# Kernel optimization log

Measured on AMD Instinct MI355X. Metric: run time of the kernel, lower is better.

## Reference

```python
import jax, jax.numpy as jnp
import numpy as np

ALPHA = 300.0   # attractor_alpha
N_ATT = 16      # n_attractors
MIN_D = 0.001
MAX_D = 10.0


def _resize_bilinear_ac(x, out_h, out_w):
    """Bilinear resize with align_corners=True on trailing (H, W) dims of [B,C,h,w]."""
    h, w = x.shape[-2], x.shape[-1]
    ys = jnp.arange(out_h, dtype=jnp.float32) * ((h - 1) / max(out_h - 1, 1))
    xs = jnp.arange(out_w, dtype=jnp.float32) * ((w - 1) / max(out_w - 1, 1))
    y0 = jnp.floor(ys).astype(jnp.int32); y1 = jnp.minimum(y0 + 1, h - 1)
    x0 = jnp.floor(xs).astype(jnp.int32); x1 = jnp.minimum(x0 + 1, w - 1)
    wy = (ys - y0.astype(jnp.float32))[:, None]   # [out_h, 1]
    wx = (xs - x0.astype(jnp.float32))[None, :]   # [1, out_w]
    v00 = x[..., y0[:, None], x0[None, :]]
    v01 = x[..., y0[:, None], x1[None, :]]
    v10 = x[..., y1[:, None], x0[None, :]]
    v11 = x[..., y1[:, None], x1[None, :]]
    top = v00 * (1 - wx) + v01 * wx
    bot = v10 * (1 - wx) + v11 * wx
    return top * (1 - wy) + bot * wy


def setup_inputs() -> dict:
    key = jax.random.key(0)
    k = jax.random.split(key, 7)
    B, C, H, W = 4, 128, 192, 192
    n_bins = 64
    x = jax.random.normal(k[0], (B, C, H, W), dtype=jnp.float32)
    prev_bin = jax.random.uniform(k[1], (B, n_bins, H // 2, W // 2), dtype=jnp.float32)
    prev_bin_embedding = jax.random.normal(k[2], (B, C, H // 2, W // 2), dtype=jnp.float32)
    w1 = jax.random.normal(k[3], (128, 128), dtype=jnp.float32) * 0.05
    b1 = jnp.zeros((128,), dtype=jnp.float32)
    w2 = jax.random.normal(k[4], (2 * N_ATT, 128), dtype=jnp.float32) * 0.05
    b2 = jnp.zeros((2 * N_ATT,), dtype=jnp.float32)
    return {"x": x, "prev_bin": prev_bin, "prev_bin_embedding": prev_bin_embedding,
            "w1": w1, "b1": b1, "w2": w2, "b2": b2}


def reference(x, prev_bin, prev_bin_embedding, w1, b1, w2, b2):
    B, C, H, W = x.shape
    # add (interpolated) previous bin embedding
    pe = _resize_bilinear_ac(prev_bin_embedding, H, W)
    h = x + pe
    # per-pixel MLP (two 1x1 convs)
    h = jax.nn.relu(jnp.einsum('bchw,oc->bohw', h, w1) + b1[:, None, None])
    att = jax.nn.relu(jnp.einsum('bchw,oc->bohw', h, w2) + b2[:, None, None]) + 0.001
    # [B, n_attractors, 2, H, W] -> take normed attractor points
    att = att.reshape(B, N_ATT, 2, H, W)[:, :, 0]          # [B, nA, H, W]
    # upsample previous bin centers to feature resolution
    bc = _resize_bilinear_ac(prev_bin, H, W)               # [B, nB, H, W]
    # broadcast-subtract + inverse attractor + mean over attractors
    dx = att[:, :, None, :, :] - bc[:, None, :, :, :]      # [B, nA, nB, H, W]
    delta_c = jnp.mean(dx / (1.0 + ALPHA * dx * dx), axis=1)  # gamma = 2
    bin_new_centers = bc + delta_c
    bin_centers = (MAX_D - MIN_D) * bin_new_centers + MIN_D
    bin_centers = jnp.clip(jnp.sort(bin_centers, axis=1), MIN_D, MAX_D)
    return bin_new_centers, bin_centers
```

## Files before the change

kernel.cpp:

```cpp
#include <hip/hip_runtime.h>

constexpr int Bc = 4, Cc = 128, Hc = 192, Wc = 192;
constexpr int HI = 96, WI = 96;
constexpr int NB = 64;
constexpr int NA = 16;
constexpr float SCL = 95.0f / 191.0f;

typedef __attribute__((ext_vector_type(8))) short bf16x8;
typedef __attribute__((ext_vector_type(4))) float f32x4;

__device__ __forceinline__ unsigned short f2bf(float f) {
  unsigned u = __builtin_bit_cast(unsigned, f);
  unsigned r = (u + 0x7FFFu + ((u >> 16) & 1u)) >> 16;
  return (unsigned short)r;
}
__device__ __forceinline__ float rcp_fast(float r) {
#if defined(__has_builtin)
#if __has_builtin(__builtin_amdgcn_rcpf)
  return __builtin_amdgcn_rcpf(r);
#else
  return 1.0f / r;
#endif
#else
  return 1.0f / r;
#endif
}

__global__ __launch_bounds__(256) void k_prep(
    const float* __restrict__ w1, const float* __restrict__ w2,
    unsigned short* __restrict__ w1p, unsigned short* __restrict__ w2p)
{
  const int t = blockIdx.x * 256 + threadIdx.x;
  if (t < 16384) {
    const int e  = t & 7;
    const int l  = (t >> 3) & 63;
    const int kt = (t >> 9) & 3;
    const int nt = t >> 11;
    const int n  = nt * 16 + (l & 15);
    const int k  = kt * 32 + (l >> 4) * 8 + e;
    w1p[t] = f2bf(w1[n * 128 + k]);
  } else {
    const int u  = t - 16384;
    const int e  = u & 7;
    const int l  = (u >> 3) & 63;
    const int kt = u >> 9;
    const int n  = 2 * (l & 15);
    const int k  = kt * 32 + (l >> 4) * 8 + e;
    w2p[u] = f2bf(w2[n * 128 + k]);
  }
}

__global__ __launch_bounds__(256, 4) void k_att(
    const float* __restrict__ x, const float* __restrict__ pbe,
    const unsigned short* __restrict__ w1p, const float* __restrict__ b1,
    const unsigned short* __restrict__ w2p, const float* __restrict__ b2,
    float* __restrict__ att)
{
  constexpr int PH = 136;
  constexpr int RP = 37;
  __shared__ __align__(16) unsigned char smem[16384 + 128 * RP * 4];
  unsigned short* w1_s  = (unsigned short*)smem;
  float*          row_s = (float*)(smem + 16384);
  unsigned short* a1_s  = (unsigned short*)(smem + 16384);

  const int tid = threadIdx.x;
  const int xg0 = blockIdx.x * 64;
  const int y = blockIdx.y;
  const int b = blockIdx.z;

  const float ysf = y * SCL;
  const int y0 = (int)ysf;
  const int y1 = min(y0 + 1, HI - 1);
  const float wy = ysf - (float)y0;
  const int xi0 = (int)(xg0 * SCL);

  const int lane = tid & 63;
  const int wv = tid >> 6;
  const int ln = lane & 15;
  const int qd = lane >> 4;
  const int m0 = wv * 16;

  const int xg = xg0 + m0 + ln;
  const float xsf = (float)xg * SCL;
  const int x0i = (int)xsf;
  const float wx = xsf - (float)x0i;
  const int xl = x0i - xi0;

  float4 wstageA[4];
  {
    const float4* wp4 = (const float4*)w1p;
    #pragma unroll
    for (int i = 0; i < 4; ++i) wstageA[i] = wp4[tid + 256 * i];
  }

  float xr[32];
  #pragma unroll
  for (int kt = 0; kt < 4; ++kt) {
    #pragma unroll
    for (int j = 0; j < 8; ++j) {
      const int c = kt * 32 + qd * 8 + j;
      xr[kt * 8 + j] = x[((size_t)(b * Cc + c) * Hc + y) * Wc + xg];
    }
  }

  #pragma unroll
  for (int i = 0; i < 18; ++i) {
    const int f = tid + 256 * i;
    const int c = f / 36;
    const int xi = f - c * 36;
    const int xgl = min(xi0 + xi, WI - 1);
    const float* p = pbe + (size_t)(b * Cc + c) * (HI * WI);
    const float top = p[y0 * WI + xgl];
    const float bot = p[y1 * WI + xgl];
    row_s[c * RP + xi] = top + wy * (bot - top);
  }

  {
    float4* ws4 = (float4*)w1_s;
    #pragma unroll
    for (int i = 0; i < 4; ++i) ws4[tid + 256 * i] = wstageA[i];
  }
  __syncthreads();

  bf16x8 af[4];
  #pragma unroll
  for (int kt = 0; kt < 4; ++kt) {
    #pragma unroll
    for (int j = 0; j < 8; ++j) {
      const int c = kt * 32 + qd * 8 + j;
      const float v0 = row_s[c * RP + xl];
      const float v1 = row_s[c * RP + xl + 1];
      af[kt][j] = (short)f2bf(xr[kt * 8 + j] + v0 + wx * (v1 - v0));
    }
  }
  __syncthreads();

  float4 wstageB[4];
  {
    const float4* wp4 = (const float4*)w1p;
    #pragma unroll
    for (int i = 0; i < 4; ++i) wstageB[i] = wp4[1024 + tid + 256 * i];
  }
  float bias1[8];
  #pragma unroll
  for (int nt = 0; nt < 8; ++nt) bias1[nt] = b1[nt * 16 + ln];

  f32x4 acc[8];
  #pragma unroll
  for (int nt = 0; nt < 8; ++nt) acc[nt] = f32x4{0.f, 0.f, 0.f, 0.f};
  #pragma unroll
  for (int nt = 0; nt < 4; ++nt) {
    #pragma unroll
    for (int kt = 0; kt < 4; ++kt) {
      const bf16x8 bf = *(const bf16x8*)&w1_s[(nt * 4 + kt) * 512 + lane * 8];
      acc[nt] = __builtin_amdgcn_mfma_f32_16x16x32_bf16(af[kt], bf, acc[nt], 0, 0, 0);
    }
  }
  #pragma unroll
  for (int nt = 0; nt < 4; ++nt) {
    const int n = nt * 16 + ln;
    const float bias = bias1[nt];
    #pragma unroll
    for (int r = 0; r < 4; ++r) {
      const int m = m0 + qd * 4 + r;
      a1_s[m * PH + n] = f2bf(fmaxf(acc[nt][r] + bias, 0.f));
    }
  }
  __syncthreads();

  {
    float4* ws4 = (float4*)w1_s;
    #pragma unroll
    for (int i = 0; i < 4; ++i) ws4[tid + 256 * i] = wstageB[i];
  }
  bf16x8 b2f[4];
  #pragma unroll
  for (int kt = 0; kt < 4; ++kt)
    b2f[kt] = *(const bf16x8*)&w2p[kt * 512 + lane * 8];
  const float bias2 = b2[2 * ln];
  __syncthreads();

  #pragma unroll
  for (int nt = 4; nt < 8; ++nt) {
    #pragma unroll
    for (int kt = 0; kt < 4; ++kt) {
      const bf16x8 bf = *(const bf16x8*)&w1_s[((nt - 4) * 4 + kt) * 512 + lane * 8];
      acc[nt] = __builtin_amdgcn_mfma_f32_16x16x32_bf16(af[kt], bf, acc[nt], 0, 0, 0);
    }
  }
  #pragma unroll
  for (int nt = 4; nt < 8; ++nt) {
    const int n = nt * 16 + ln;
    const float bias = bias1[nt];
    #pragma unroll
    for (int r = 0; r < 4; ++r) {
      const int m = m0 + qd * 4 + r;
      a1_s[m * PH + n] = f2bf(fmaxf(acc[nt][r] + bias, 0.f));
    }
  }

  f32x4 acc2 = f32x4{0.f, 0.f, 0.f, 0.f};
  #pragma unroll
  for (int kt = 0; kt < 4; ++kt) {
    const bf16x8 a2 = *(const bf16x8*)&a1_s[(m0 + ln) * PH + kt * 32 + qd * 8];
    acc2 = __builtin_amdgcn_mfma_f32_16x16x32_bf16(a2, b2f[kt], acc2, 0, 0, 0);
  }
  #pragma unroll
  for (int r = 0; r < 4; ++r) {
    const int opx = m0 + qd * 4 + r;
    const float v = fmaxf(acc2[r] + bias2, 0.f) + 0.001f;
    att[((size_t)((b * Hc + y) * Wc) + xg0 + opx) * NA + ln] = v;
  }
}

__global__ __launch_bounds__(192, 6) void k_bins(
    const float* __restrict__ pb, const float* __restrict__ att,
    float* __restrict__ out0, float* __restrict__ out1)
{
  constexpr int PW = 51;
  __shared__ __align__(16) float smem2[NB * PW];
  float* pbrow = smem2;
  float* xch   = smem2;

  const int tid = threadIdx.x;
  const int y  = blockIdx.x;
  const int b  = blockIdx.y;
  const int hx = blockIdx.z;

  const int h  = (tid >= 96) ? 1 : 0;
  const int p  = tid - 96 * h;
  const int px = 96 * hx + p;

  const float ysf = y * SCL;
  const int y0 = (int)ysf;
  const int y1 = min(y0 + 1, HI - 1);
  const float wy = ysf - (float)y0;

  const int xi0 = hx ? 47 : 0;

  float am[16];
  {
    const float4* ap = (const float4*)(att + ((size_t)((b * Hc + y) * Wc) + px) * NA);
    const float4 a0 = ap[0], a1 = ap[1], a2 = ap[2], a3 = ap[3];
    am[0] = a0.x;  am[1] = a0.y;  am[2] = a0.z;  am[3] = a0.w;
    am[4] = a1.x;  am[5] = a1.y;  am[6] = a1.z;  am[7] = a1.w;
    am[8] = a2.x;  am[9] = a2.y;  am[10] = a2.z; am[11] = a2.w;
    am[12] = a3.x; am[13] = a3.y; am[14] = a3.z; am[15] = a3.w;
  }

  #pragma unroll
  for (int i = 0; i < 17; ++i) {
    const int u = tid + 192 * i;
    if (u < 3200) {
      const int k = u / 50;
      const int xi = u - k * 50;
      const int xs = min(xi0 + xi, WI - 1);
      const float* base = pb + (size_t)(b * NB + k) * (HI * WI);
      const float top = base[y0 * WI + xs];
      const float bot = base[y1 * WI + xs];
      pbrow[k * PW + xi] = top + wy * (bot - top);
    }
  }
  __syncthreads();

  const float xsf = px * SCL;
  const int x0 = (int)xsf;
  const float wx = xsf - (float)x0;
  const int xl = x0 - xi0;

  const size_t obase = (size_t)(b * NB) * (Hc * Wc) + (size_t)y * Wc + px;
  float v[32];

  #pragma unroll
  for (int kb = 0; kb < 32; kb += 4) {
    float bc[4], dl[4];
    #pragma unroll
    for (int q = 0; q < 4; ++q) {
      const int k = h * 32 + kb + q;
      const float v0 = pbrow[k * PW + xl], v1 = pbrow[k * PW + xl + 1];
      bc[q] = v0 + wx * (v1 - v0);
      dl[q] = 0.f;
    }
    #pragma unroll
    for (int j = 0; j < NA; ++j) {
      const float a = am[j];
      #pragma unroll
      for (int q = 0; q < 4; ++q) {
        const float d = a - bc[q];
        const float rq = fmaf(300.f * d, d, 1.f);
        dl[q] = fmaf(d, rcp_fast(rq), dl[q]);
      }
    }
    #pragma unroll
    for (int q = 0; q < 4; ++q) {
      const float bnc = fmaf(dl[q], 1.f / 16.f, bc[q]);
      out0[obase + (size_t)(h * 32 + kb + q) * (Hc * Wc)] = bnc;
      v[kb + q] = fmaf(9.999f, bnc, 0.001f);
    }
  }

  #pragma unroll
  for (int size = 2; size <= 32; size <<= 1) {
    #pragma unroll
    for (int stride = size >> 1; stride >= 1; stride >>= 1) {
      #pragma unroll
      for (int i = 0; i < 32; ++i) {
        if ((i & stride) == 0) {
          const int j = i | stride;
          const bool asc = (((i & size) == 0) != (h == 1));
          const float a = v[i], c = v[j];
          const float lo = fminf(a, c), hi = fmaxf(a, c);
          v[i] = asc ? lo : hi;
          v[j] = asc ? hi : lo;
        }
      }
    }
  }

  __syncthreads();
  if (h) {
    #pragma unroll
    for (int i = 0; i < 32; ++i) xch[i * 96 + p] = v[i];
  }
  __syncthreads();
  if (!h) {
    #pragma unroll
    for (int i = 0; i < 32; ++i) {
      const float o = xch[i * 96 + p];
      const float mn = fminf(v[i], o), mx = fmaxf(v[i], o);
      v[i] = mn;
      xch[i * 96 + p] = mx;
    }
  }
  __syncthreads();
  if (h) {
    #pragma unroll
    for (int i = 0; i < 32; ++i) v[i] = xch[i * 96 + p];
  }

  #pragma unroll
  for (int stride = 16; stride >= 1; stride >>= 1) {
    #pragma unroll
    for (int i = 0; i < 32; ++i) {
      if ((i & stride) == 0) {
        const int j = i | stride;
        const float a = v[i], c = v[j];
        v[i] = fminf(a, c);
        v[j] = fmaxf(a, c);
      }
    }
  }

  #pragma unroll
  for (int i = 0; i < 32; ++i) {
    out1[obase + (size_t)(h * 32 + i) * (Hc * Wc)] =
        fminf(fmaxf(v[i], 0.001f), 10.0f);
  }
}

extern "C" void kernel_launch(void* const* d_in, const int* in_sizes, int n_in,
                              void* d_out, int out_size, void* d_ws, size_t ws_size,
                              hipStream_t stream) {
  const float* x   = (const float*)d_in[0];
  const float* pb  = (const float*)d_in[1];
  const float* pbe = (const float*)d_in[2];
  const float* w1  = (const float*)d_in[3];
  const float* b1  = (const float*)d_in[4];
  const float* w2  = (const float*)d_in[5];
  const float* b2  = (const float*)d_in[6];

  float* out0 = (float*)d_out;
  float* out1 = out0 + (size_t)Bc * NB * Hc * Wc;

  unsigned short* w1p = (unsigned short*)d_ws;
  unsigned short* w2p = w1p + 16384;
  float* att = (float*)((char*)d_ws + 65536);

  k_prep<<<72, 256, 0, stream>>>(w1, w2, w1p, w2p);

  dim3 g1(Wc / 64, Hc, Bc);
  k_att<<<g1, 256, 0, stream>>>(x, pbe, w1p, b1, w2p, b2, att);

  dim3 g2(Hc, Bc, 2);
  k_bins<<<g2, 192, 0, stream>>>(pb, att, out0, out1);
}
```

Measured before the change: 235.6 us.

## Stage full W1 in LDS once and vectorize prev_bin row loads

k_att now stages all of W1 (32KB bf16) in shared memory up front instead of in two halves. This removes two barriers and the mid-kernel reload, and the W2 fragments and biases are now loaded early. The larger LDS footprint lowers the occupancy hint from 4 to 3 blocks. k_bins loads prev_bin rows as 16-byte-aligned float4 vectors (13 groups of 4 at offset 0 or 44) instead of scalar loads, with the row pitch padded to 56. It clamps the right neighbour index and lowers its occupancy hint to 4.

Result: faster. 215.1 us (-8.7%).

```diff
diff --git a/kernel.cpp b/kernel.cpp
--- a/kernel.cpp
+++ b/kernel.cpp
@@ -50,7 +50,7 @@
   }
 }
 
-__global__ __launch_bounds__(256, 4) void k_att(
+__global__ __launch_bounds__(256, 3) void k_att(
     const float* __restrict__ x, const float* __restrict__ pbe,
     const unsigned short* __restrict__ w1p, const float* __restrict__ b1,
     const unsigned short* __restrict__ w2p, const float* __restrict__ b2,
@@ -58,10 +58,10 @@
 {
   constexpr int PH = 136;
   constexpr int RP = 37;
-  __shared__ __align__(16) unsigned char smem[16384 + 128 * RP * 4];
+  __shared__ __align__(16) unsigned char smem[32768 + 128 * RP * 4];
   unsigned short* w1_s  = (unsigned short*)smem;
-  float*          row_s = (float*)(smem + 16384);
-  unsigned short* a1_s  = (unsigned short*)(smem + 16384);
+  float*          row_s = (float*)(smem + 32768);
+  unsigned short* a1_s  = (unsigned short*)(smem + 32768);
 
   const int tid = threadIdx.x;
   const int xg0 = blockIdx.x * 64;
@@ -86,12 +86,21 @@
   const float wx = xsf - (float)x0i;
   const int xl = x0i - xi0;
 
-  float4 wstageA[4];
+  float4 wstage[8];
   {
     const float4* wp4 = (const float4*)w1p;
     #pragma unroll
-    for (int i = 0; i < 4; ++i) wstageA[i] = wp4[tid + 256 * i];
-  }
+    for (int i = 0; i < 8; ++i) wstage[i] = wp4[tid + 256 * i];
+  }
+
+  bf16x8 b2f[4];
+  #pragma unroll
+  for (int kt = 0; kt < 4; ++kt)
+    b2f[kt] = *(const bf16x8*)&w2p[kt * 512 + lane * 8];
+  float bias1[8];
+  #pragma unroll
+  for (int nt = 0; nt < 8; ++nt) bias1[nt] = b1[nt * 16 + ln];
+  const float bias2 = b2[2 * ln];
 
   float xr[32];
   #pragma unroll
@@ -118,7 +127,7 @@
   {
     float4* ws4 = (float4*)w1_s;
     #pragma unroll
-    for (int i = 0; i < 4; ++i) ws4[tid + 256 * i] = wstageA[i];
+    for (int i = 0; i < 8; ++i) ws4[tid + 256 * i] = wstage[i];
   }
   __syncthreads();
 
@@ -135,61 +144,20 @@
   }
   __syncthreads();
 
-  float4 wstageB[4];
-  {
-    const float4* wp4 = (const float4*)w1p;
-    #pragma unroll
-    for (int i = 0; i < 4; ++i) wstageB[i] = wp4[1024 + tid + 256 * i];
-  }
-  float bias1[8];
-  #pragma unroll
-  for (int nt = 0; nt < 8; ++nt) bias1[nt] = b1[nt * 16 + ln];
-
   f32x4 acc[8];
   #pragma unroll
   for (int nt = 0; nt < 8; ++nt) acc[nt] = f32x4{0.f, 0.f, 0.f, 0.f};
   #pragma unroll
-  for (int nt = 0; nt < 4; ++nt) {
+  for (int nt = 0; nt < 8; ++nt) {
     #pragma unroll
     for (int kt = 0; kt < 4; ++kt) {
       const bf16x8 bf = *(const bf16x8*)&w1_s[(nt * 4 + kt) * 512 + lane * 8];
       acc[nt] = __builtin_amdgcn_mfma_f32_16x16x32_bf16(af[kt], bf, acc[nt], 0, 0, 0);
     }
   }
-  #pragma unroll
-  for (int nt = 0; nt < 4; ++nt) {
-    const int n = nt * 16 + ln;
-    const float bias = bias1[nt];
-    #pragma unroll
-    for (int r = 0; r < 4; ++r) {
-      const int m = m0 + qd * 4 + r;
-      a1_s[m * PH + n] = f2bf(fmaxf(acc[nt][r] + bias, 0.f));
-    }
-  }
-  __syncthreads();
-
-  {
-    float4* ws4 = (float4*)w1_s;
-    #pragma unroll
-    for (int i = 0; i < 4; ++i) ws4[tid + 256 * i] = wstageB[i];
-  }
-  bf16x8 b2f[4];
-  #pragma unroll
-  for (int kt = 0; kt < 4; ++kt)
-    b2f[kt] = *(const bf16x8*)&w2p[kt * 512 + lane * 8];
-  const float bias2 = b2[2 * ln];
-  __syncthreads();
-
-  #pragma unroll
-  for (int nt = 4; nt < 8; ++nt) {
-    #pragma unroll
-    for (int kt = 0; kt < 4; ++kt) {
-      const bf16x8 bf = *(const bf16x8*)&w1_s[((nt - 4) * 4 + kt) * 512 + lane * 8];
-      acc[nt] = __builtin_amdgcn_mfma_f32_16x16x32_bf16(af[kt], bf, acc[nt], 0, 0, 0);
-    }
-  }
-  #pragma unroll
-  for (int nt = 4; nt < 8; ++nt) {
+
+  #pragma unroll
+  for (int nt = 0; nt < 8; ++nt) {
     const int n = nt * 16 + ln;
     const float bias = bias1[nt];
     #pragma unroll
@@ -213,11 +181,11 @@
   }
 }
 
-__global__ __launch_bounds__(192, 6) void k_bins(
+__global__ __launch_bounds__(192, 4) void k_bins(
     const float* __restrict__ pb, const float* __restrict__ att,
     float* __restrict__ out0, float* __restrict__ out1)
 {
-  constexpr int PW = 51;
+  constexpr int PW = 56;
   __shared__ __align__(16) float smem2[NB * PW];
   float* pbrow = smem2;
   float* xch   = smem2;
@@ -236,7 +204,7 @@
   const int y1 = min(y0 + 1, HI - 1);
   const float wy = ysf - (float)y0;
 
-  const int xi0 = hx ? 47 : 0;
+  const int xb = hx ? 44 : 0;
 
   float am[16];
   {
@@ -249,16 +217,20 @@
   }
 
   #pragma unroll
-  for (int i = 0; i < 17; ++i) {
+  for (int i = 0; i < 5; ++i) {
     const int u = tid + 192 * i;
-    if (u < 3200) {
-      const int k = u / 50;
-      const int xi = u - k * 50;
-      const int xs = min(xi0 + xi, WI - 1);
+    if (u < 832) {
+      const int k = u / 13;
+      const int g = u - k * 13;
       const float* base = pb + (size_t)(b * NB + k) * (HI * WI);
-      const float top = base[y0 * WI + xs];
-      const float bot = base[y1 * WI + xs];
-      pbrow[k * PW + xi] = top + wy * (bot - top);
+      const float4 t4 = *(const float4*)&base[y0 * WI + xb + g * 4];
+      const float4 b4 = *(const float4*)&base[y1 * WI + xb + g * 4];
+      float4 r;
+      r.x = t4.x + wy * (b4.x - t4.x);
+      r.y = t4.y + wy * (b4.y - t4.y);
+      r.z = t4.z + wy * (b4.z - t4.z);
+      r.w = t4.w + wy * (b4.w - t4.w);
+      *(float4*)&pbrow[k * PW + g * 4] = r;
     }
   }
   __syncthreads();
@@ -266,7 +238,8 @@
   const float xsf = px * SCL;
   const int x0 = (int)xsf;
   const float wx = xsf - (float)x0;
-  const int xl = x0 - xi0;
+  const int xl = x0 - xb;
+  const int i1 = min(xl + 1, 51);
 
   const size_t obase = (size_t)(b * NB) * (Hc * Wc) + (size_t)y * Wc + px;
   float v[32];
@@ -277,7 +250,7 @@
     #pragma unroll
     for (int q = 0; q < 4; ++q) {
       const int k = h * 32 + kb + q;
-      const float v0 = pbrow[k * PW + xl], v1 = pbrow[k * PW + xl + 1];
+      const float v0 = pbrow[k * PW + xl], v1 = pbrow[k * PW + i1];
       bc[q] = v0 + wx * (v1 - v0);
       dl[q] = 0.f;
     }
```
